# Performance work log

Measured on AMD Instinct MI355X. Metric: run time of the kernel, lower is better.

Reference implementation:

```python
import jax, jax.numpy as jnp
import numpy as np

B, C, H, W = 8, 384, 32, 32
NUM_HEADS = 8
HEAD_DIM = C // NUM_HEADS


def setup_inputs() -> dict:
    key = jax.random.key(0)
    k1, k2, k3, k4, k5 = jax.random.split(key, 5)
    s = 1.0 / np.sqrt(C)
    return {
        "x": jax.random.normal(k1, (B, C, H, W), dtype=jnp.float32),
        "w_qkv": jax.random.normal(k2, (3 * C, C), dtype=jnp.float32) * s,   # 1x1 conv == linear over channels
        "b_qkv": jax.random.normal(k3, (3 * C,), dtype=jnp.float32) * 0.01,
        "w_proj": jax.random.normal(k4, (C, C), dtype=jnp.float32) * s,
        "b_proj": jax.random.normal(k5, (C,), dtype=jnp.float32) * 0.01,
    }


def reference(x, w_qkv, b_qkv, w_proj, b_proj):
    b, c, h, w = x.shape
    n = h * w
    scale = HEAD_DIM ** (-0.5)
    # 1x1 conv qkv: (B, 3C, H, W)
    qkv = jnp.einsum('bchw,oc->bohw', x, w_qkv) + b_qkv[None, :, None, None]
    # 'b (three hd d) h0 w0 -> three b hd (h0 w0) d'
    qkv = qkv.reshape(b, 3, NUM_HEADS, HEAD_DIM, n)
    qkv = jnp.transpose(qkv, (1, 0, 2, 4, 3))  # (3, B, heads, N, d)
    q, k, v = qkv[0], qkv[1], qkv[2]
    attn = jnp.einsum('bhnd,bhmd->bhnm', q, k) * scale
    attn = jax.nn.softmax(attn, axis=-1)
    out = jnp.einsum('bhnm,bhmd->bhnd', attn, v)          # (B, heads, N, d)
    out = jnp.transpose(out, (0, 1, 3, 2)).reshape(b, c, h, w)  # b (hd d) h w
    out = jnp.einsum('bchw,oc->bohw', out, w_proj) + b_proj[None, :, None, None]
    return out
```

## Files before the change

### kernel.cpp

```cpp
#include <hip/hip_runtime.h>
#include <hip/hip_bf16.h>

typedef __hip_bfloat16 bf16;
typedef __bf16 bfx8 __attribute__((ext_vector_type(8)));
typedef float f32x4 __attribute__((ext_vector_type(4)));

#define Bk   8
#define Ck   384
#define NHk  8
#define Dk   48
#define Dp   64
#define Nk   1024
#define O3   1152


__device__ __forceinline__ void gload_lds16(const bf16* src, void* dst)
{
    __builtin_amdgcn_global_load_lds(
        (const __attribute__((address_space(1))) void*)src,
        (__attribute__((address_space(3))) void*)dst, 16, 0, 0);
}

__device__ __forceinline__ int pack2(float a, float b)
{
    bf16 ha = __float2bfloat16(a), hb = __float2bfloat16(b);
    unsigned lo = *(unsigned short*)&ha, hi = *(unsigned short*)&hb;
    return (int)(lo | (hi << 16));
}

__device__ __forceinline__ ushort4 pack4(float v0, float v1, float v2, float v3)
{
    bf16 h0 = __float2bfloat16(v0), h1 = __float2bfloat16(v1);
    bf16 h2 = __float2bfloat16(v2), h3 = __float2bfloat16(v3);
    ushort4 pk;
    pk.x = *(unsigned short*)&h0; pk.y = *(unsigned short*)&h1;
    pk.z = *(unsigned short*)&h2; pk.w = *(unsigned short*)&h3;
    return pk;
}

__global__ __launch_bounds__(256) void prep_kernel(
    const float* __restrict__ x, bf16* __restrict__ Xs,
    const float* __restrict__ wq, const float* __restrict__ wp,
    bf16* __restrict__ Wq, bf16* __restrict__ Wp,
    bf16* __restrict__ Qs, bf16* __restrict__ Ks)
{
    const int u = blockIdx.x * 256 + threadIdx.x;
    if (u < 393216) {
        int n = u & 1023, rest = u >> 10;
        int oct = rest % 48, b = rest / 48;
        const float* xb = x + (size_t)b * Ck * Nk;
        float f[8];
        #pragma unroll
        for (int e = 0; e < 8; ++e) f[e] = xb[(size_t)(oct * 8 + e) * Nk + n];
        int4 v = { pack2(f[0], f[1]), pack2(f[2], f[3]),
                   pack2(f[4], f[5]), pack2(f[6], f[7]) };
        bf16* dst = Xs + ((size_t)b * 64 + (n >> 4)) * 6144 + oct * 128 + (n & 15) * 8;
        *(int4*)dst = v;
    } else if (u < 448512) {
        int u1 = u - 393216;
        int o = u1 % 1152, oct = u1 / 1152;
        const float* src = wq + (size_t)o * Ck + oct * 8;
        int4 v = { pack2(src[0], src[1]), pack2(src[2], src[3]),
                   pack2(src[4], src[5]), pack2(src[6], src[7]) };
        bf16* dst = Wq + ((size_t)(o >> 4) * 48 + oct) * 128 + (o & 15) * 8;
        *(int4*)dst = v;
    } else if (u < 466944) {
        int u2 = u - 448512;
        int o = u2 % 384, oct = u2 / 384;
        const float* src = wp + (size_t)o * Ck + oct * 8;
        int4 v = { pack2(src[0], src[1]), pack2(src[2], src[3]),
                   pack2(src[4], src[5]), pack2(src[6], src[7]) };
        bf16* dst = Wp + ((size_t)(o >> 4) * 48 + oct) * 128 + (o & 15) * 8;
        *(int4*)dst = v;
    } else {
        int i = u - 466944;
        int buf = i >> 17;
        int r17 = i & 131071;
        int head = r17 >> 11;
        int r11 = r17 & 2047;
        int g = r11 >> 5, c5 = r11 & 31;
        int cd = 6 + (c5 >> 4), e = c5 & 15;
        bf16* p = (buf ? Ks : Qs) + (size_t)head * 65536 +
                  ((size_t)g * 8 + cd) * 128 + e * 8;
        *(int4*)p = (int4){0, 0, 0, 0};
    }
}

__global__ __launch_bounds__(256, 2) void qkv_mfma_kernel(
    const bf16* __restrict__ Xs, const bf16* __restrict__ Wq,
    const float* __restrict__ bias,
    bf16* __restrict__ Qs, bf16* __restrict__ Ks, bf16* __restrict__ Vs)
{
    __shared__ __align__(16) bf16 Wl[24576];

    const int b    = blockIdx.x;
    const int by   = blockIdx.y;
    const int bx   = blockIdx.z;
    const int o0   = by * 64;
    const int n0   = bx * 256;
    const int wave = threadIdx.x >> 6;
    const int lane = threadIdx.x & 63;
    const int l15  = lane & 15, quad = lane >> 4;
    const int t3   = o0 / Ck;

    {
        const bf16* wsrc = Wq + (size_t)by * 24576;
        #pragma unroll
        for (int i = 0; i < 12; ++i) {
            int f = wave * 12 + i;
            gload_lds16(wsrc + f * 512 + lane * 8, (char*)Wl + f * 1024);
        }
    }

    const bf16* xg[4];
    #pragma unroll
    for (int i = 0; i < 4; ++i)
        xg[i] = Xs + ((size_t)(b * 64 + bx * 16 + wave * 4 + i) * 48) * 128 + lane * 8;
    const bf16* wl = Wl + lane * 8;

    bfx8 fx0[4];
    #pragma unroll
    for (int i = 0; i < 4; ++i) fx0[i] = *(const bfx8*)(xg[i]);

    f32x4 acc[16];
    #pragma unroll
    for (int i = 0; i < 16; ++i) acc[i] = (f32x4){0.f, 0.f, 0.f, 0.f};

    asm volatile("s_waitcnt vmcnt(0)" ::: "memory");
    __syncthreads();

    if (t3 < 2) {
        #pragma unroll
        for (int s = 0; s < 12; ++s) {
            bfx8 fx[4], fw[4];
            #pragma unroll
            for (int i = 0; i < 4; ++i)
                fx[i] = (s == 0) ? fx0[i] : *(const bfx8*)(xg[i] + s * 512);
            #pragma unroll
            for (int j = 0; j < 4; ++j) fw[j] = *(const bfx8*)(wl + j * 6144 + s * 512);
            #pragma unroll
            for (int j = 0; j < 4; ++j)
                #pragma unroll
                for (int i = 0; i < 4; ++i)
                    acc[j * 4 + i] = __builtin_amdgcn_mfma_f32_16x16x32_bf16(
                        fw[j], fx[i], acc[j * 4 + i], 0, 0, 0);
        }
        const float qscale = 0.2082350964f;
        #pragma unroll
        for (int j = 0; j < 4; ++j) {
            int ob = o0 + j * 16 + quad * 4;
            float4 bi = *(const float4*)&bias[ob];
            int r  = ob - t3 * Ck;
            int hd = r / Dk, d0 = r - hd * Dk;
            bf16* hb = (t3 == 0 ? Qs : Ks) + (size_t)(b * NHk + hd) * 65536
                     + (d0 >> 3) * 128 + (d0 & 7);
            #pragma unroll
            for (int i = 0; i < 4; ++i) {
                int npos = n0 + wave * 64 + i * 16 + l15;
                f32x4 a = acc[j * 4 + i];
                float v0 = a[0] + bi.x, v1 = a[1] + bi.y;
                float v2 = a[2] + bi.z, v3 = a[3] + bi.w;
                if (t3 == 0) { v0 *= qscale; v1 *= qscale; v2 *= qscale; v3 *= qscale; }
                *(ushort4*)(hb + (size_t)(npos >> 4) * 1024 + (npos & 15) * 8) =
                    pack4(v0, v1, v2, v3);
            }
        }
    } else {
        #pragma unroll
        for (int s = 0; s < 12; ++s) {
            bfx8 fx[4], fw[4];
            #pragma unroll
            for (int i = 0; i < 4; ++i)
                fx[i] = (s == 0) ? fx0[i] : *(const bfx8*)(xg[i] + s * 512);
            #pragma unroll
            for (int j = 0; j < 4; ++j) fw[j] = *(const bfx8*)(wl + j * 6144 + s * 512);
            #pragma unroll
            for (int i = 0; i < 4; ++i)
                #pragma unroll
                for (int j = 0; j < 4; ++j)
                    acc[i * 4 + j] = __builtin_amdgcn_mfma_f32_16x16x32_bf16(
                        fx[i], fw[j], acc[i * 4 + j], 0, 0, 0);
        }
        #pragma unroll
        for (int j = 0; j < 4; ++j) {
            int ov = o0 + j * 16 + l15;
            float bi = bias[ov];
            int r  = ov - 2 * Ck;
            int hd = r / Dk, d = r - hd * Dk;
            bf16* vbp = Vs + (size_t)(b * NHk + hd) * 49152
                      + (size_t)(d >> 4) * 16384 + (d & 15) * 8;
            #pragma unroll
            for (int i = 0; i < 4; ++i) {
                int npb = n0 + wave * 64 + i * 16 + quad * 4;
                f32x4 a = acc[i * 4 + j];
                *(ushort4*)(vbp + (size_t)(npb >> 3) * 128 + (npb & 7)) =
                    pack4(a[0] + bi, a[1] + bi, a[2] + bi, a[3] + bi);
            }
        }
    }
}

__global__ __launch_bounds__(256, 2) void attn_kernel(
    const bf16* __restrict__ Qs, const bf16* __restrict__ Ks,
    const bf16* __restrict__ Vs, bf16* __restrict__ AO)
{
    __shared__ __align__(16) bf16 KbL[3][4096];
    __shared__ __align__(16) bf16 VbL[3][3072];
    __shared__ __align__(16) short Ps[4 * 2304];
    __shared__ float sums[4][2][16];

    const int hd   = blockIdx.x;
    const int b    = blockIdx.y;
    const int bx   = blockIdx.z;
    const int t    = threadIdx.x;
    const int wave = t >> 6;
    const int lane = t & 63;
    const int l15  = lane & 15;
    const int quad = lane >> 4;
    const int grp16 = (bx * 4 + wave) * 2;

    const bf16* qb = Qs + (size_t)(b * NHk + hd) * 65536;
    const bf16* kb = Ks + (size_t)(b * NHk + hd) * 65536;
    const bf16* vb = Vs + (size_t)(b * NHk + hd) * 49152;

    auto stage = [&](int slot, int k0) {
        const bf16* ksrc = kb + (size_t)k0 * 64;
        const bf16* vsrc = vb + (size_t)(k0 >> 3) * 128;
        char* kdst = (char*)&KbL[slot][0];
        char* vdst = (char*)&VbL[slot][0];
        #pragma unroll
        for (int i = 0; i < 4; ++i) {
            const int l = wave + i * 4;
            if (l < 14) {
                const int piece = l >> 1, half = l & 1;
                const bf16* src; char* dst;
                if (piece < 4) {
                    src = ksrc + piece * 1024 + half * 512 + lane * 8;
                    dst = kdst + piece * 2048 + half * 1024;
                } else {
                    const int dc = piece - 4;
                    src = vsrc + (size_t)dc * 16384 + half * 512 + lane * 8;
                    dst = vdst + dc * 2048 + half * 1024;
                }
                gload_lds16(src, dst);
            }
        }
    };

    stage(0, 0);
    stage(1, 64);

    bfx8 bq[2][2];
    #pragma unroll
    for (int qt = 0; qt < 2; ++qt) {
        const bf16* qp = qb + ((size_t)(grp16 + qt) * 8 + quad) * 128 + l15 * 8;
        bq[qt][0] = *(const bfx8*)(qp);
        bq[qt][1] = *(const bfx8*)(qp + 512);
    }

    float l_run[2] = {0.f, 0.f};
    f32x4 oacc[2][3];
    #pragma unroll
    for (int qt = 0; qt < 2; ++qt)
        #pragma unroll
        for (int dc = 0; dc < 3; ++dc) oacc[qt][dc] = (f32x4){0.f, 0.f, 0.f, 0.f};

    short* const PsW[2] = { Ps + wave * 2304, Ps + wave * 2304 + 1152 };
    const int lo = quad * 128 + l15 * 8;

    #pragma unroll 1
    for (int c = 0; c < 16; ++c) {
        if (c < 15) {
            if (wave < 2) asm volatile("s_waitcnt vmcnt(4)" ::: "memory");
            else          asm volatile("s_waitcnt vmcnt(3)" ::: "memory");
        } else {
            asm volatile("s_waitcnt vmcnt(0)" ::: "memory");
        }
        __builtin_amdgcn_sched_barrier(0);
        __builtin_amdgcn_s_barrier();
        __builtin_amdgcn_sched_barrier(0);

        const int slot = c % 3;
        const bf16* Kc = &KbL[slot][0];
        const bf16* Vc = &VbL[slot][0];

        f32x4 sf[2][4];
        __builtin_amdgcn_s_setprio(1);
        #pragma unroll
        for (int s = 0; s < 4; ++s) {
            const bfx8 kf0 = *(const bfx8*)(Kc + s * 1024 + lo);
            const bfx8 kf1 = *(const bfx8*)(Kc + s * 1024 + 512 + lo);
            #pragma unroll
            for (int qt = 0; qt < 2; ++qt) {
                f32x4 z = (f32x4){0.f, 0.f, 0.f, 0.f};
                z = __builtin_amdgcn_mfma_f32_16x16x32_bf16(kf0, bq[qt][0], z, 0, 0, 0);
                z = __builtin_amdgcn_mfma_f32_16x16x32_bf16(kf1, bq[qt][1], z, 0, 0, 0);
                sf[qt][s] = z;
            }
        }
        __builtin_amdgcn_s_setprio(0);

        #pragma unroll
        for (int qt = 0; qt < 2; ++qt) {
            float lsum = 0.f;
            #pragma unroll
            for (int s = 0; s < 4; ++s) {
                float e0 = __builtin_amdgcn_exp2f(sf[qt][s][0]);
                float e1 = __builtin_amdgcn_exp2f(sf[qt][s][1]);
                float e2 = __builtin_amdgcn_exp2f(sf[qt][s][2]);
                float e3 = __builtin_amdgcn_exp2f(sf[qt][s][3]);
                lsum += (e0 + e1) + (e2 + e3);
                *(ushort4*)&PsW[qt][l15 * 72 + s * 16 + quad * 4] =
                    pack4(e0, e1, e2, e3);
            }
            l_run[qt] += lsum;
        }

        __builtin_amdgcn_s_setprio(1);
        #pragma unroll
        for (int qt = 0; qt < 2; ++qt) {
            const bfx8 ap0 = *(const bfx8*)&PsW[qt][l15 * 72 + quad * 8];
            const bfx8 ap1 = *(const bfx8*)&PsW[qt][l15 * 72 + 32 + quad * 8];
            #pragma unroll
            for (int dc = 0; dc < 3; ++dc) {
                const bfx8 bv0 = *(const bfx8*)(Vc + dc * 1024 + lo);
                const bfx8 bv1 = *(const bfx8*)(Vc + dc * 1024 + 512 + lo);
                oacc[qt][dc] = __builtin_amdgcn_mfma_f32_16x16x32_bf16(
                    ap0, bv0, oacc[qt][dc], 0, 0, 0);
                oacc[qt][dc] = __builtin_amdgcn_mfma_f32_16x16x32_bf16(
                    ap1, bv1, oacc[qt][dc], 0, 0, 0);
            }
        }
        __builtin_amdgcn_s_setprio(0);

        if (c + 2 < 16) stage((c + 2) % 3, (c + 2) * 64);
    }

    #pragma unroll
    for (int qt = 0; qt < 2; ++qt) {
        float lt = l_run[qt];
        lt += __shfl_xor(lt, 16, 64);
        lt += __shfl_xor(lt, 32, 64);
        sums[wave][qt][l15] = lt;
    }
    asm volatile("s_waitcnt lgkmcnt(0)" ::: "memory");

    #pragma unroll
    for (int qt = 0; qt < 2; ++qt) {
        short* OsW = PsW[qt];
        #pragma unroll
        for (int r = 0; r < 4; ++r) {
            int qi = quad * 4 + r;
            float rli = 1.0f / sums[wave][qt][qi];
            #pragma unroll
            for (int dcc = 0; dcc < 3; ++dcc) {
                bf16 hb = __float2bfloat16(oacc[qt][dcc][r] * rli);
                OsW[qi * 64 + dcc * 16 + l15] = *(short*)&hb;
            }
        }
    }
    asm volatile("s_waitcnt lgkmcnt(0)" ::: "memory");

    #pragma unroll
    for (int qt = 0; qt < 2; ++qt) {
        bf16* aob = AO + (((size_t)b * 64 + grp16 + qt) * 48 + hd * 6) * 128;
        short* OsW = PsW[qt];
        int u = lane;
        int4 v = *(const int4*)&OsW[(u & 15) * 64 + (u >> 4) * 8];
        *(int4*)(aob + u * 8) = v;
        if (lane < 32) {
            int u2 = 64 + lane;
            int4 v2 = *(const int4*)&OsW[(u2 & 15) * 64 + (u2 >> 4) * 8];
            *(int4*)(aob + u2 * 8) = v2;
        }
    }
}

__global__ __launch_bounds__(256, 2) void proj_mfma_kernel(
    const bf16* __restrict__ AO, const bf16* __restrict__ Wp,
    const float* __restrict__ bias, float* __restrict__ out)
{
    __shared__ __align__(16) bf16 Wl[24576];

    const int b    = blockIdx.x;
    const int by   = blockIdx.y;
    const int bx   = blockIdx.z;
    const int o0   = by * 64;
    const int n0   = bx * 256;
    const int wave = threadIdx.x >> 6;
    const int lane = threadIdx.x & 63;
    const int l15  = lane & 15, quad = lane >> 4;

    {
        const bf16* wsrc = Wp + (size_t)by * 24576;
        #pragma unroll
        for (int i = 0; i < 12; ++i) {
            int f = wave * 12 + i;
            gload_lds16(wsrc + f * 512 + lane * 8, (char*)Wl + f * 1024);
        }
    }

    const bf16* ag[4];
    #pragma unroll
    for (int i = 0; i < 4; ++i)
        ag[i] = AO + ((size_t)(b * 64 + bx * 16 + wave * 4 + i) * 48) * 128 + lane * 8;
    const bf16* wl = Wl + lane * 8;

    bfx8 fx0[4];
    #pragma unroll
    for (int i = 0; i < 4; ++i) fx0[i] = *(const bfx8*)(ag[i]);

    f32x4 acc[16];
    #pragma unroll
    for (int i = 0; i < 16; ++i) acc[i] = (f32x4){0.f, 0.f, 0.f, 0.f};

    asm volatile("s_waitcnt vmcnt(0)" ::: "memory");
    __syncthreads();

    #pragma unroll
    for (int s = 0; s < 12; ++s) {
        bfx8 fx[4], fw[4];
        #pragma unroll
        for (int i = 0; i < 4; ++i)
            fx[i] = (s == 0) ? fx0[i] : *(const bfx8*)(ag[i] + s * 512);
        #pragma unroll
        for (int j = 0; j < 4; ++j) fw[j] = *(const bfx8*)(wl + j * 6144 + s * 512);
        #pragma unroll
        for (int i = 0; i < 4; ++i)
            #pragma unroll
            for (int j = 0; j < 4; ++j)
                acc[i * 4 + j] = __builtin_amdgcn_mfma_f32_16x16x32_bf16(
                    fx[i], fw[j], acc[i * 4 + j], 0, 0, 0);
    }

    #pragma unroll
    for (int j = 0; j < 4; ++j) {
        int o = o0 + j * 16 + l15;
        float bi = bias[o];
        #pragma unroll
        for (int i = 0; i < 4; ++i) {
            int npb = n0 + wave * 64 + i * 16 + quad * 4;
            f32x4 a = acc[i * 4 + j];
            float4 v = { a[0] + bi, a[1] + bi, a[2] + bi, a[3] + bi };
            *(float4*)&out[((size_t)b * Ck + o) * Nk + npb] = v;
        }
    }
}

extern "C" void kernel_launch(void* const* d_in, const int* in_sizes, int n_in,
                              void* d_out, int out_size, void* d_ws, size_t ws_size,
                              hipStream_t stream)
{
    const float* x      = (const float*)d_in[0];
    const float* w_qkv  = (const float*)d_in[1];
    const float* b_qkv  = (const float*)d_in[2];
    const float* w_proj = (const float*)d_in[3];
    const float* b_proj = (const float*)d_in[4];
    float* out = (float*)d_out;

    const size_t XT_SEG = (size_t)Bk * Nk * Ck;
    const size_t WQ_SEG = (size_t)O3 * Ck;
    const size_t WP_SEG = (size_t)Ck * Ck;
    const size_t QK_SEG = (size_t)Bk * NHk * Nk * Dp;
    const size_t V_SEG  = (size_t)Bk * NHk * Dk * Nk;

    bf16* Xs = (bf16*)d_ws;
    bf16* Wq = Xs + XT_SEG;
    bf16* Wp = Wq + WQ_SEG;
    bf16* Qs = Wp + WP_SEG;
    bf16* Ks = Qs + QK_SEG;
    bf16* Vs = Ks + QK_SEG;
    bf16* AO = Vs + V_SEG;

    prep_kernel<<<2848, 256, 0, stream>>>(x, Xs, w_qkv, w_proj, Wq, Wp, Qs, Ks);
    qkv_mfma_kernel<<<dim3(Bk, 18, 4), 256, 0, stream>>>(
        Xs, Wq, b_qkv, Qs, Ks, Vs);
    attn_kernel<<<dim3(NHk, Bk, 8), 256, 0, stream>>>(Qs, Ks, Vs, AO);
    proj_mfma_kernel<<<dim3(Bk, 6, 4), 256, 0, stream>>>(
        AO, Wp, b_proj, out);
}
```

Before: 124.1 us.

## Switch attention K/V staging from triple to double buffering with unrolled pairs

Replaces the three-slot LDS ring with fine-grained vmcnt waits by a two-buffer ping-pong. The prefetch of the next chunk is issued at the start of each step, and a full vmcnt(0) wait plus barrier comes at the end. It also drops the s_setprio hints and swaps the grid order so batch is the fastest block index. This cuts LDS use, which may allow more resident blocks, but shortens the prefetch distance, so load latency may be exposed.

Result: no change. 122.7 us (-1.1%).

```diff
diff --git a/kernel.cpp b/kernel.cpp
--- a/kernel.cpp
+++ b/kernel.cpp
@@ -204,13 +204,13 @@
     const bf16* __restrict__ Qs, const bf16* __restrict__ Ks,
     const bf16* __restrict__ Vs, bf16* __restrict__ AO)
 {
-    __shared__ __align__(16) bf16 KbL[3][4096];
-    __shared__ __align__(16) bf16 VbL[3][3072];
-    __shared__ __align__(16) short Ps[4 * 2304];
+    __shared__ __align__(16) bf16 KbL[2][4096];
+    __shared__ __align__(16) bf16 VbL[2][3072];
+    __shared__ __align__(16) short Ps[4 * 2 * 1152];
     __shared__ float sums[4][2][16];
 
-    const int hd   = blockIdx.x;
-    const int b    = blockIdx.y;
+    const int b    = blockIdx.x;
+    const int hd   = blockIdx.y;
     const int bx   = blockIdx.z;
     const int t    = threadIdx.x;
     const int wave = t >> 6;
@@ -223,11 +223,11 @@
     const bf16* kb = Ks + (size_t)(b * NHk + hd) * 65536;
     const bf16* vb = Vs + (size_t)(b * NHk + hd) * 49152;
 
-    auto stage = [&](int slot, int k0) {
+    auto stage = [&](int buf, int k0) {
         const bf16* ksrc = kb + (size_t)k0 * 64;
         const bf16* vsrc = vb + (size_t)(k0 >> 3) * 128;
-        char* kdst = (char*)&KbL[slot][0];
-        char* vdst = (char*)&VbL[slot][0];
+        char* kdst = (char*)&KbL[buf][0];
+        char* vdst = (char*)&VbL[buf][0];
         #pragma unroll
         for (int i = 0; i < 4; ++i) {
             const int l = wave + i * 4;
@@ -248,7 +248,6 @@
     };
 
     stage(0, 0);
-    stage(1, 64);
 
     bfx8 bq[2][2];
     #pragma unroll
@@ -268,24 +267,16 @@
     short* const PsW[2] = { Ps + wave * 2304, Ps + wave * 2304 + 1152 };
     const int lo = quad * 128 + l15 * 8;
 
-    #pragma unroll 1
-    for (int c = 0; c < 16; ++c) {
-        if (c < 15) {
-            if (wave < 2) asm volatile("s_waitcnt vmcnt(4)" ::: "memory");
-            else          asm volatile("s_waitcnt vmcnt(3)" ::: "memory");
-        } else {
-            asm volatile("s_waitcnt vmcnt(0)" ::: "memory");
-        }
-        __builtin_amdgcn_sched_barrier(0);
-        __builtin_amdgcn_s_barrier();
-        __builtin_amdgcn_sched_barrier(0);
-
-        const int slot = c % 3;
-        const bf16* Kc = &KbL[slot][0];
-        const bf16* Vc = &VbL[slot][0];
+    asm volatile("s_waitcnt vmcnt(0)" ::: "memory");
+    __syncthreads();
+
+    auto step = [&](int buf, int k0, bool pf) {
+        if (pf) stage(buf ^ 1, k0 + 64);
+
+        const bf16* Kc = &KbL[buf][0];
+        const bf16* Vc = &VbL[buf][0];
 
         f32x4 sf[2][4];
-        __builtin_amdgcn_s_setprio(1);
         #pragma unroll
         for (int s = 0; s < 4; ++s) {
             const bfx8 kf0 = *(const bfx8*)(Kc + s * 1024 + lo);
@@ -298,7 +289,6 @@
                 sf[qt][s] = z;
             }
         }
-        __builtin_amdgcn_s_setprio(0);
 
         #pragma unroll
         for (int qt = 0; qt < 2; ++qt) {
@@ -316,7 +306,6 @@
             l_run[qt] += lsum;
         }
 
-        __builtin_amdgcn_s_setprio(1);
         #pragma unroll
         for (int qt = 0; qt < 2; ++qt) {
             const bfx8 ap0 = *(const bfx8*)&PsW[qt][l15 * 72 + quad * 8];
@@ -331,9 +320,15 @@
                     ap1, bv1, oacc[qt][dc], 0, 0, 0);
             }
         }
-        __builtin_amdgcn_s_setprio(0);
-
-        if (c + 2 < 16) stage((c + 2) % 3, (c + 2) * 64);
+
+        asm volatile("s_waitcnt vmcnt(0)" ::: "memory");
+        __syncthreads();
+    };
+
+    #pragma unroll 1
+    for (int k0 = 0; k0 < Nk; k0 += 128) {
+        step(0, k0, true);
+        step(1, k0 + 64, k0 + 128 < Nk);
     }
 
     #pragma unroll
@@ -475,7 +470,7 @@
     prep_kernel<<<2848, 256, 0, stream>>>(x, Xs, w_qkv, w_proj, Wq, Wp, Qs, Ks);
     qkv_mfma_kernel<<<dim3(Bk, 18, 4), 256, 0, stream>>>(
         Xs, Wq, b_qkv, Qs, Ks, Vs);
-    attn_kernel<<<dim3(NHk, Bk, 8), 256, 0, stream>>>(Qs, Ks, Vs, AO);
+    attn_kernel<<<dim3(Bk, NHk, 8), 256, 0, stream>>>(Qs, Ks, Vs, AO);
     proj_mfma_kernel<<<dim3(Bk, 6, 4), 256, 0, stream>>>(
         AO, Wp, b_proj, out);
 }
```
